# Optimization experiments

Measured on AMD Instinct MI355X. Metric: run time of the kernel, lower is better.

The kernel has to match this reference:

```python
import jax, jax.numpy as jnp
import numpy as np

SEQ, BATCH, HIDDEN = 4096, 16, 512


def setup_inputs() -> dict:
    key = jax.random.key(0)
    ks = jax.random.split(key, 8)
    scale = 1.0 / np.sqrt(HIDDEN)
    outputs_hidden = jax.random.normal(ks[0], (1, BATCH, HIDDEN), jnp.float32)
    encoder_out = jax.random.normal(ks[1], (SEQ, BATCH, HIDDEN), jnp.float32)
    encoder_features = jax.random.normal(ks[2], (SEQ, BATCH, HIDDEN), jnp.float32)
    # binary-ish float mask, mostly ones
    encoder_mask = (jax.random.uniform(ks[3], (BATCH, 1, SEQ)) > 0.1).astype(jnp.float32)
    # running sum of positive exp-scores; keep strictly positive
    temporal_scores_sum = jax.random.uniform(ks[4], (BATCH, 1, SEQ)) + 0.5
    W_feat = jax.random.normal(ks[5], (HIDDEN, HIDDEN), jnp.float32) * scale
    b_feat = jax.random.normal(ks[6], (HIDDEN,), jnp.float32)
    v_attn = jax.random.normal(ks[7], (HIDDEN,), jnp.float32) * scale
    return {
        "outputs_hidden": outputs_hidden,
        "encoder_out": encoder_out,
        "encoder_features": encoder_features,
        "encoder_mask": encoder_mask,
        "temporal_scores_sum": temporal_scores_sum,
        "W_feat": W_feat,
        "b_feat": b_feat,
        "v_attn": v_attn,
    }


def reference(outputs_hidden, encoder_out, encoder_features, encoder_mask,
              temporal_scores_sum, W_feat, b_feat, v_attn):
    # self.features: Linear(hidden, hidden) on decoder state [1, b, h]
    decoder_features = jnp.einsum('obh,kh->obk', outputs_hidden, W_feat) + b_feat
    # additive score: tanh(dec + enc) . v  -> [s, b]
    scores = jnp.einsum('sbh,h->sb', jnp.tanh(decoder_features + encoder_features), v_attn)
    # Permute(1,2,0) of [s,b,1] -> [b,1,s], then exp
    temporal_attention = jnp.exp(scores).T[:, None, :]  # [b, 1, s]
    attention = temporal_attention / temporal_scores_sum
    new_scores_sum = temporal_attention + temporal_scores_sum
    attention = attention * encoder_mask
    attention = attention / jnp.sum(attention, axis=-1, keepdims=True)  # Normalize(-1)
    enc = jnp.transpose(encoder_out, (1, 0, 2))           # [b, s, h]
    context = jnp.matmul(attention, enc)                  # [b, 1, h]
    context = jnp.transpose(context, (1, 0, 2))           # [1, b, h]
    return context, attention, new_scores_sum
```

## Files before the change

### kernel.cpp

```cpp
#include <hip/hip_runtime.h>
#include <hip/hip_bf16.h>
#include <stdint.h>

#define SEQ 4096
#define BATCH 16
#define HID 512
#define ATT_OFF (BATCH * HID)
#define NSS_OFF (BATCH * HID + BATCH * SEQ)
#define SPB 64
#define NCHUNK (SEQ / SPB)
#define SPW (SPB / 4)

typedef unsigned short u16;
typedef unsigned int u32;

__device__ __forceinline__ float bflo(u32 w) { return __uint_as_float(w << 16); }
__device__ __forceinline__ float bfhi(u32 w) { return __uint_as_float(w & 0xffff0000u); }

__device__ __forceinline__ u16 f2bf(float f) {
  u32 u = __float_as_uint(f);
  return (u16)((u + 0x7fffu + ((u >> 16) & 1u)) >> 16);
}

__device__ __forceinline__ int probe_bf16(const void* tssp) {
  const u16* t = (const u16*)tssp;
  int ok = 1;
  #pragma unroll
  for (int i = 0; i < 8; i += 2) {
    u16 u = t[i];
    ok &= (u >= 0x3F00 && u <= 0x3FC0) ? 1 : 0;
  }
  return ok;
}

template <int BF>
__device__ __forceinline__ float ld1(const void* p, size_t i) {
  if (BF) return __uint_as_float(((u32)((const u16*)p)[i]) << 16);
  return ((const float*)p)[i];
}

template <int BF>
__device__ __forceinline__ void st1(void* p, size_t i, float v) {
  if (BF) ((u16*)p)[i] = f2bf(v);
  else    ((float*)p)[i] = v;
}

template <int BF>
__device__ __forceinline__ void load8(const void* p, size_t e, float* o) {
  if (BF) {
    uint4 v = *(const uint4*)((const u16*)p + e);
    o[0]=bflo(v.x); o[1]=bfhi(v.x); o[2]=bflo(v.y); o[3]=bfhi(v.y);
    o[4]=bflo(v.z); o[5]=bfhi(v.z); o[6]=bflo(v.w); o[7]=bfhi(v.w);
  } else {
    const float4* f = (const float4*)((const float*)p + e);
    float4 a = f[0], b = f[1];
    o[0]=a.x; o[1]=a.y; o[2]=a.z; o[3]=a.w;
    o[4]=b.x; o[5]=b.y; o[6]=b.z; o[7]=b.w;
  }
}

__device__ __forceinline__ float fast_tanh(float x) {
  float e = __expf(2.0f * x);
  return 1.0f - 2.0f * __builtin_amdgcn_rcpf(e + 1.0f);
}

__device__ __forceinline__ float wave_sum(float acc) {
  #pragma unroll
  for (int off = 32; off; off >>= 1) acc += __shfl_xor(acc, off, 64);
  return acc;
}

template <int BF>
__device__ __forceinline__ void k_dec_body(
    const void* oh, const void* W, const void* bias, float* dec) {
  int tid = threadIdx.x;
  int gw = blockIdx.x * 4 + (tid >> 6);
  int lane = tid & 63;
  int k = gw & (HID - 1);
  int b = gw >> 9;
  float wv[8], ov[8];
  load8<BF>(W,  (size_t)k * HID + lane * 8, wv);
  load8<BF>(oh, (size_t)b * HID + lane * 8, ov);
  float acc = 0.0f;
  #pragma unroll
  for (int j = 0; j < 8; ++j) acc += wv[j] * ov[j];
  acc = wave_sum(acc);
  if (lane == 0) dec[b * HID + k] = acc + ld1<BF>(bias, k);
}

__global__ __launch_bounds__(256) void k_dec(
    const void* oh, const void* W, const void* bias, const void* tss,
    float* dec, float* denom) {
  if (blockIdx.x == 0 && threadIdx.x < BATCH) denom[threadIdx.x] = 0.0f;
  if (probe_bf16(tss)) k_dec_body<1>(oh, W, bias, dec);
  else                 k_dec_body<0>(oh, W, bias, dec);
}

template <int BF>
__device__ __forceinline__ void k_fused_body(
    const void* ef, const void* eo, const void* maskp, const void* tssp,
    const void* vp, const float* dec, float* w_buf, float* denom,
    float* partial, void* out) {
  int tid = threadIdx.x, lane = tid & 63, wave = tid >> 6;
  int blk = blockIdx.x;
  int b = blk >> 6;
  int chunk = blk & (NCHUNK - 1);
  int s0 = chunk * SPB + wave * SPW;
  float dv[8], vv[8];
  #pragma unroll
  for (int j = 0; j < 8; ++j) dv[j] = dec[b * HID + lane * 8 + j];
  load8<BF>(vp, lane * 8, vv);
  float a[8] = {0,0,0,0,0,0,0,0};
  float wsum = 0.0f;
  for (int i = 0; i < SPW; ++i) {
    int s = s0 + i;
    size_t rowoff = ((size_t)s * BATCH + b) * HID + lane * 8;
    float ev[8];
    load8<BF>(ef, rowoff, ev);
    float eov[8];
    load8<BF>(eo, rowoff, eov);
    float acc = 0.0f;
    #pragma unroll
    for (int j = 0; j < 8; ++j) acc += fast_tanh(ev[j] + dv[j]) * vv[j];
    acc = wave_sum(acc);
    float p  = __expf(acc);
    float ts = ld1<BF>(tssp,  b * SEQ + s);
    float m  = ld1<BF>(maskp, b * SEQ + s);
    float w  = p * m * __builtin_amdgcn_rcpf(ts);
    if (lane == 0) {
      st1<BF>(out, NSS_OFF + b * SEQ + s, p + ts);
      w_buf[b * SEQ + s] = w;
      wsum += w;
    }
    #pragma unroll
    for (int j = 0; j < 8; ++j) a[j] += w * eov[j];
  }
  __shared__ float red[3 * 64 * 8];
  __shared__ float wpart[4];
  if (lane == 0) wpart[wave] = wsum;
  if (wave > 0) {
    float* r = &red[(((wave - 1) * 64) + lane) * 8];
    #pragma unroll
    for (int j = 0; j < 8; ++j) r[j] = a[j];
  }
  __syncthreads();
  if (wave == 0) {
    #pragma unroll
    for (int k = 0; k < 3; ++k) {
      const float* r = &red[((k * 64) + lane) * 8];
      #pragma unroll
      for (int j = 0; j < 8; ++j) a[j] += r[j];
    }
    float4* p4 = (float4*)(partial + ((size_t)b * NCHUNK + chunk) * HID + lane * 8);
    p4[0] = make_float4(a[0], a[1], a[2], a[3]);
    p4[1] = make_float4(a[4], a[5], a[6], a[7]);
    if (tid == 0)
      atomicAdd(&denom[b], wpart[0] + wpart[1] + wpart[2] + wpart[3]);
  }
}

__global__ __launch_bounds__(256) void k_fused(
    const void* ef, const void* eo, const void* maskp, const void* tssp,
    const void* vp, const float* dec, float* w_buf, float* denom,
    float* partial, void* out) {
  if (probe_bf16(tssp))
    k_fused_body<1>(ef, eo, maskp, tssp, vp, dec, w_buf, denom, partial, out);
  else
    k_fused_body<0>(ef, eo, maskp, tssp, vp, dec, w_buf, denom, partial, out);
}

template <int BF>
__device__ __forceinline__ void k_fin_body(
    const float* w_buf, const float* denom, const float* partial, void* out) {
  int b = blockIdx.x;
  int tid = threadIdx.x;
  float inv_d = __builtin_amdgcn_rcpf(denom[b]);
  #pragma unroll
  for (int k = 0; k < SEQ / 256; ++k) {
    int s = k * 256 + tid;
    st1<BF>(out, ATT_OFF + b * SEQ + s, w_buf[b * SEQ + s] * inv_d);
  }
  #pragma unroll
  for (int r = 0; r < HID / 256; ++r) {
    int h = r * 256 + tid;
    float sum = 0.0f;
    for (int c = 0; c < NCHUNK; ++c)
      sum += partial[((size_t)b * NCHUNK + c) * HID + h];
    st1<BF>(out, b * HID + h, sum * inv_d);
  }
}

__global__ __launch_bounds__(256) void k_finalize(
    const float* w_buf, const float* denom, const float* partial,
    const void* tssp, void* out) {
  if (probe_bf16(tssp)) k_fin_body<1>(w_buf, denom, partial, out);
  else                  k_fin_body<0>(w_buf, denom, partial, out);
}

extern "C" void kernel_launch(void* const* d_in, const int* in_sizes, int n_in,
                              void* d_out, int out_size, void* d_ws, size_t ws_size,
                              hipStream_t stream) {
  const void* oh   = d_in[0];
  const void* eo   = d_in[1];
  const void* ef   = d_in[2];
  const void* mask = d_in[3];
  const void* tss  = d_in[4];
  const void* W    = d_in[5];
  const void* bias = d_in[6];
  const void* v    = d_in[7];

  float* ws      = (float*)d_ws;
  float* dec     = ws;
  float* w_buf   = dec + BATCH * HID;
  float* denom   = w_buf + BATCH * SEQ;
  float* partial = denom + 16;

  k_dec     <<<2048, 256, 0, stream>>>(oh, W, bias, tss, dec, denom);
  k_fused   <<<1024, 256, 0, stream>>>(ef, eo, mask, tss, v, dec, w_buf,
                                       denom, partial, d_out);
  k_finalize<<<  16, 256, 0, stream>>>(w_buf, denom, partial, tss, d_out);
}
```

Baseline: 308.2 us.

## Batch score reductions, double fused grid, and parallelize finalize across more blocks

Halves the sequence chunk per block so the fused kernel launches twice as many blocks. Inside each wave, all score rows are loaded and reduced together with interleaved shuffles, and the encoder_out loads are moved into a separate pass so more memory requests are in flight. The LDS reduction layout becomes lane-contiguous to avoid bank conflicts. The finalize kernel is split across 8 blocks per batch, but the doubled chunk count doubles the partial buffer it must sum.

```diff
diff --git a/kernel.cpp b/kernel.cpp
--- a/kernel.cpp
+++ b/kernel.cpp
@@ -7,7 +7,7 @@
 #define HID 512
 #define ATT_OFF (BATCH * HID)
 #define NSS_OFF (BATCH * HID + BATCH * SEQ)
-#define SPB 64
+#define SPB 32
 #define NCHUNK (SEQ / SPB)
 #define SPW (SPB / 4)
 
@@ -62,12 +62,6 @@
 __device__ __forceinline__ float fast_tanh(float x) {
   float e = __expf(2.0f * x);
   return 1.0f - 2.0f * __builtin_amdgcn_rcpf(e + 1.0f);
-}
-
-__device__ __forceinline__ float wave_sum(float acc) {
-  #pragma unroll
-  for (int off = 32; off; off >>= 1) acc += __shfl_xor(acc, off, 64);
-  return acc;
 }
 
 template <int BF>
@@ -84,7 +78,8 @@
   float acc = 0.0f;
   #pragma unroll
   for (int j = 0; j < 8; ++j) acc += wv[j] * ov[j];
-  acc = wave_sum(acc);
+  #pragma unroll
+  for (int off = 32; off; off >>= 1) acc += __shfl_xor(acc, off, 64);
   if (lane == 0) dec[b * HID + k] = acc + ld1<BF>(bias, k);
 }
 
@@ -103,54 +98,65 @@
     float* partial, void* out) {
   int tid = threadIdx.x, lane = tid & 63, wave = tid >> 6;
   int blk = blockIdx.x;
-  int b = blk >> 6;
+  int b = blk >> 7;
   int chunk = blk & (NCHUNK - 1);
   int s0 = chunk * SPB + wave * SPW;
   float dv[8], vv[8];
   #pragma unroll
   for (int j = 0; j < 8; ++j) dv[j] = dec[b * HID + lane * 8 + j];
   load8<BF>(vp, lane * 8, vv);
-  float a[8] = {0,0,0,0,0,0,0,0};
+
+  float acc[SPW];
+  #pragma unroll
+  for (int i = 0; i < SPW; ++i) {
+    float ev[8];
+    load8<BF>(ef, ((size_t)(s0 + i) * BATCH + b) * HID + lane * 8, ev);
+    float s = 0.0f;
+    #pragma unroll
+    for (int j = 0; j < 8; ++j) s += fast_tanh(ev[j] + dv[j]) * vv[j];
+    acc[i] = s;
+  }
+  #pragma unroll
+  for (int off = 32; off; off >>= 1) {
+    #pragma unroll
+    for (int i = 0; i < SPW; ++i) acc[i] += __shfl_xor(acc[i], off, 64);
+  }
+  float w[SPW];
   float wsum = 0.0f;
+  #pragma unroll
   for (int i = 0; i < SPW; ++i) {
     int s = s0 + i;
-    size_t rowoff = ((size_t)s * BATCH + b) * HID + lane * 8;
-    float ev[8];
-    load8<BF>(ef, rowoff, ev);
-    float eov[8];
-    load8<BF>(eo, rowoff, eov);
-    float acc = 0.0f;
-    #pragma unroll
-    for (int j = 0; j < 8; ++j) acc += fast_tanh(ev[j] + dv[j]) * vv[j];
-    acc = wave_sum(acc);
-    float p  = __expf(acc);
+    float p  = __expf(acc[i]);
     float ts = ld1<BF>(tssp,  b * SEQ + s);
     float m  = ld1<BF>(maskp, b * SEQ + s);
-    float w  = p * m * __builtin_amdgcn_rcpf(ts);
+    w[i] = p * m * __builtin_amdgcn_rcpf(ts);
+    wsum += w[i];
     if (lane == 0) {
       st1<BF>(out, NSS_OFF + b * SEQ + s, p + ts);
-      w_buf[b * SEQ + s] = w;
-      wsum += w;
+      w_buf[b * SEQ + s] = w[i];
     }
-    #pragma unroll
-    for (int j = 0; j < 8; ++j) a[j] += w * eov[j];
-  }
-  __shared__ float red[3 * 64 * 8];
+  }
+  float a[8] = {0,0,0,0,0,0,0,0};
+  #pragma unroll
+  for (int i = 0; i < SPW; ++i) {
+    float eov[8];
+    load8<BF>(eo, ((size_t)(s0 + i) * BATCH + b) * HID + lane * 8, eov);
+    #pragma unroll
+    for (int j = 0; j < 8; ++j) a[j] += w[i] * eov[j];
+  }
+  __shared__ float red[3 * 8 * 64];
   __shared__ float wpart[4];
   if (lane == 0) wpart[wave] = wsum;
   if (wave > 0) {
-    float* r = &red[(((wave - 1) * 64) + lane) * 8];
-    #pragma unroll
-    for (int j = 0; j < 8; ++j) r[j] = a[j];
+    #pragma unroll
+    for (int j = 0; j < 8; ++j) red[((wave - 1) * 8 + j) * 64 + lane] = a[j];
   }
   __syncthreads();
   if (wave == 0) {
     #pragma unroll
-    for (int k = 0; k < 3; ++k) {
-      const float* r = &red[((k * 64) + lane) * 8];
+    for (int k = 0; k < 3; ++k)
       #pragma unroll
-      for (int j = 0; j < 8; ++j) a[j] += r[j];
-    }
+      for (int j = 0; j < 8; ++j) a[j] += red[(k * 8 + j) * 64 + lane];
     float4* p4 = (float4*)(partial + ((size_t)b * NCHUNK + chunk) * HID + lane * 8);
     p4[0] = make_float4(a[0], a[1], a[2], a[3]);
     p4[1] = make_float4(a[4], a[5], a[6], a[7]);
@@ -172,17 +178,17 @@
 template <int BF>
 __device__ __forceinline__ void k_fin_body(
     const float* w_buf, const float* denom, const float* partial, void* out) {
-  int b = blockIdx.x;
+  int b = blockIdx.x >> 3;
+  int part = blockIdx.x & 7;
   int tid = threadIdx.x;
   float inv_d = __builtin_amdgcn_rcpf(denom[b]);
   #pragma unroll
-  for (int k = 0; k < SEQ / 256; ++k) {
-    int s = k * 256 + tid;
+  for (int k = 0; k < 2; ++k) {
+    int s = part * 512 + k * 256 + tid;
     st1<BF>(out, ATT_OFF + b * SEQ + s, w_buf[b * SEQ + s] * inv_d);
   }
-  #pragma unroll
-  for (int r = 0; r < HID / 256; ++r) {
-    int h = r * 256 + tid;
+  if (tid < 64) {
+    int h = part * 64 + tid;
     float sum = 0.0f;
     for (int c = 0; c < NCHUNK; ++c)
       sum += partial[((size_t)b * NCHUNK + c) * HID + h];
@@ -216,7 +222,7 @@
   float* partial = denom + 16;
 
   k_dec     <<<2048, 256, 0, stream>>>(oh, W, bias, tss, dec, denom);
-  k_fused   <<<1024, 256, 0, stream>>>(ef, eo, mask, tss, v, dec, w_buf,
+  k_fused   <<<2048, 256, 0, stream>>>(ef, eo, mask, tss, v, dec, w_buf,
                                        denom, partial, d_out);
-  k_finalize<<<  16, 256, 0, stream>>>(w_buf, denom, partial, tss, d_out);
-}
+  k_finalize<<< 128, 256, 0, stream>>>(w_buf, denom, partial, tss, d_out);
+}
```

New measurement: 301.9 us. 1.02x faster.
